# Kernel optimization log

Hardware: AMD Instinct MI355X
Metric: run time of the kernel (lower is better)

The kernel has to match this reference:

```python
import jax, jax.numpy as jnp
import numpy as np

DIM = 20
N = 200000
E = 6400000
ITERATIONS = 3


def setup_inputs() -> dict:
    key = jax.random.key(0)
    ks = jax.random.split(key, 20)
    inp = {
        "h": jax.random.normal(ks[0], (N, DIM), dtype=jnp.float32),
        "node2depth": jax.random.randint(ks[1], (N,), 0, 5, dtype=jnp.int32),
        "edge_src": jax.random.randint(ks[2], (E,), 0, N, dtype=jnp.int32),
        "edge_dst": jax.random.randint(ks[3], (E,), 0, N, dtype=jnp.int32),
    }
    # Six DIM x DIM Linear layers (weight stored [out,in] like torch, plus bias)
    scale = 1.0 / np.sqrt(DIM)
    names = ["Wz", "Uz", "Wr", "Ur", "Wh", "Uh"]
    for j, nm in enumerate(names):
        inp[nm + "_w"] = jax.random.uniform(ks[4 + 2 * j], (DIM, DIM), jnp.float32, -scale, scale)
        inp[nm + "_b"] = jax.random.uniform(ks[5 + 2 * j], (DIM,), jnp.float32, -scale, scale)
    return inp


def _linear(x, w, b):
    return x @ w.T + b


def reference(h, Wz_w, Wz_b, Uz_w, Uz_b, Wr_w, Wr_b, Ur_w, Ur_b,
              Wh_w, Wh_b, Uh_w, Uh_b, node2depth, edge_src, edge_dst):
    active = None
    for i in range(ITERATIONS):
        # active set shrinks as i grows (depth + i <= ITERATIONS)
        active = (node2depth + i) <= ITERATIONS  # [N] bool
        af = active.astype(h.dtype)
        # x[u] = sum over neighbors v of h[v], counting only active src AND active dst
        msg = h[edge_src] * af[edge_src][:, None]          # [E, DIM]
        x = jax.ops.segment_sum(msg, edge_dst, num_segments=N)  # [N, DIM]
        x = x * af[:, None]
        z = jax.nn.sigmoid(_linear(x, Wz_w, Wz_b) + _linear(h, Uz_w, Uz_b))
        r = jax.nn.sigmoid(_linear(x, Wr_w, Wr_b) + _linear(h, Ur_w, Ur_b))
        h_cand = jnp.tanh(_linear(x, Wh_w, Wh_b) + _linear(r * h, Uh_w, Uh_b))
        h_new = z * h + (1.0 - z) * h_cand
        # inactive nodes are dropped from the dict in the original; since the
        # active set only shrinks, keeping their old h is equivalent
        h = jnp.where(active[:, None], h_new, h)
    # original returns only nodes active at the last iteration; zero out the rest
    return jnp.where(active[:, None], h, jnp.zeros_like(h))
```

## Files before the change

kernel.cpp:

```cpp
#include <hip/hip_runtime.h>

#define DIM    20
#define NN     200000
#define EE     6400000
#define ITERS  3
#define BLOCK  256

#define NODES_PER_FINE   64
#define NFINE            3125
#define NCOARSE          98
#define FINE_PER_COARSE  32
#define TILE             4096
#define IPT              16
#define XSTRIDE          21
#define NBINS            2560

typedef unsigned int u32;

__global__ __launch_bounds__(BLOCK) void k1_count(const int* __restrict__ edst,
                                                  int* __restrict__ fine_cnt) {
    __shared__ u32 lhist[NFINE];
    int tid = threadIdx.x;
    for (int i = tid; i < NFINE; i += BLOCK) lhist[i] = 0;
    __syncthreads();
    for (int e = blockIdx.x * BLOCK + tid; e < EE; e += gridDim.x * BLOCK) {
        int d = edst[e];
        atomicAdd(&lhist[d >> 6], 1u);
    }
    __syncthreads();
    for (int i = tid; i < NFINE; i += BLOCK) {
        u32 v = lhist[i];
        if (v) atomicAdd((u32*)&fine_cnt[i], v);
    }
}

__global__ __launch_bounds__(BLOCK) void k2_scan(const int* __restrict__ fine_cnt,
                                                 int* __restrict__ fine_base,
                                                 int* __restrict__ fine_cursor,
                                                 int* __restrict__ coarse_base,
                                                 int* __restrict__ coarse_cursor) {
    const int CH = 13;
    int tid = threadIdx.x;
    int loc[CH];
    int base = tid * CH;
    int s = 0;
    #pragma unroll
    for (int j = 0; j < CH; ++j) {
        int idx = base + j;
        int v = (idx < NFINE) ? fine_cnt[idx] : 0;
        loc[j] = v; s += v;
    }
    __shared__ int wsum[4];
    int lane = tid & 63, wid = tid >> 6;
    int incl = s;
    #pragma unroll
    for (int off = 1; off < 64; off <<= 1) {
        int t = __shfl_up(incl, off, 64);
        if (lane >= off) incl += t;
    }
    if (lane == 63) wsum[wid] = incl;
    __syncthreads();
    int woff = 0;
    for (int w = 0; w < wid; ++w) woff += wsum[w];
    int run = woff + incl - s;
    #pragma unroll
    for (int j = 0; j < CH; ++j) {
        int idx = base + j;
        if (idx < NFINE) {
            fine_base[idx]   = run;
            fine_cursor[idx] = run;
            run += loc[j];
        }
    }
    if (tid == 0) fine_base[NFINE] = EE;
    __syncthreads();
    if (tid < NCOARSE + 1) {
        int f = tid * FINE_PER_COARSE; if (f > NFINE) f = NFINE;
        int v = fine_base[f];
        coarse_base[tid] = v;
        if (tid < NCOARSE) coarse_cursor[tid] = v;
    }
}

__global__ __launch_bounds__(BLOCK) void p1_split(const int* __restrict__ esrc,
                                                  const int* __restrict__ edst,
                                                  const int* __restrict__ depth,
                                                  int* __restrict__ coarse_cursor,
                                                  u32* __restrict__ buf1) {
    __shared__ u32 lhist[NCOARSE];
    __shared__ u32 gbase[NCOARSE];
    int tid = threadIdx.x;
    int start = blockIdx.x * TILE;
    if (tid < NCOARSE) lhist[tid] = 0;
    __syncthreads();

    u32 item[IPT]; u32 key[IPT]; u32 rank[IPT];
    #pragma unroll
    for (int k = 0; k < IPT; ++k) {
        int e = start + k * BLOCK + tid;
        if (e < EE) {
            int d = edst[e];
            int s = esrc[e];
            u32 dep = (u32)depth[s];
            u32 c = (u32)d >> 11;
            key[k]  = c;
            item[k] = ((u32)d & 2047u) | ((u32)s << 11) | (dep << 29);
            rank[k] = atomicAdd(&lhist[c], 1u);
        }
    }
    __syncthreads();
    if (tid < NCOARSE) {
        u32 cnt = lhist[tid];
        gbase[tid] = cnt ? (u32)atomicAdd((u32*)&coarse_cursor[tid], cnt) : 0u;
    }
    __syncthreads();
    #pragma unroll
    for (int k = 0; k < IPT; ++k) {
        int e = start + k * BLOCK + tid;
        if (e < EE) buf1[gbase[key[k]] + rank[k]] = item[k];
    }
}

__global__ __launch_bounds__(BLOCK) void p2_split(const u32* __restrict__ buf1,
                                                  const int* __restrict__ coarse_base,
                                                  int* __restrict__ fine_cursor,
                                                  u32* __restrict__ buf2) {
    __shared__ u32 lhist[2 * FINE_PER_COARSE];
    __shared__ u32 gbase[2 * FINE_PER_COARSE];
    __shared__ int cb[NCOARSE + 1];
    __shared__ int sc0;
    int tid = threadIdx.x;
    int start = blockIdx.x * TILE;
    if (tid < NCOARSE + 1) cb[tid] = coarse_base[tid];
    if (tid < 2 * FINE_PER_COARSE) { lhist[tid] = 0; gbase[tid] = 0; }
    __syncthreads();
    if (tid == 0) {
        int c = 0;
        while (c + 1 < NCOARSE && cb[c + 1] <= start) ++c;
        sc0 = c;
    }
    __syncthreads();
    int c0 = sc0;
    int b1 = cb[c0 + 1];

    u32 item[IPT]; u32 key[IPT]; u32 rank[IPT];
    #pragma unroll
    for (int k = 0; k < IPT; ++k) {
        int i = start + k * BLOCK + tid;
        if (i < EE) {
            u32 w = buf1[i];
            u32 dlow = w & 2047u;
            u32 sdep = w >> 11;
            u32 kk = ((i < b1) ? 0u : (u32)FINE_PER_COARSE) + (dlow >> 6);
            key[k]  = kk;
            item[k] = (dlow & 63u) | (sdep << 6);
            rank[k] = atomicAdd(&lhist[kk], 1u);
        }
    }
    __syncthreads();
    if (tid < 2 * FINE_PER_COARSE) {
        u32 cnt = lhist[tid];
        int idx = c0 * FINE_PER_COARSE + tid;
        if (cnt && idx < NFINE)
            gbase[tid] = (u32)atomicAdd((u32*)&fine_cursor[idx], cnt);
    }
    __syncthreads();
    #pragma unroll
    for (int k = 0; k < IPT; ++k) {
        int i = start + k * BLOCK + tid;
        if (i < EE) buf2[gbase[key[k]] + rank[k]] = item[k];
    }
}

__global__ __launch_bounds__(BLOCK) void pb_sort(const u32* __restrict__ buf2,
                                                 const int* __restrict__ fine_base,
                                                 int* __restrict__ ptr,
                                                 u32* __restrict__ cnt3,
                                                 u32* __restrict__ ssrc) {
    __shared__ u32 hist[NBINS];
    __shared__ u32 ebase[NBINS];
    __shared__ u32 lout[TILE];
    __shared__ u32 wsum[4];
    int tid = threadIdx.x;
    int b = blockIdx.x;
    int lo = fine_base[b];
    int hi = fine_base[b + 1];
    int cnt = hi - lo;
    for (int i = tid; i < NBINS; i += BLOCK) hist[i] = 0;
    __syncthreads();

    u32 item[IPT]; u32 key[IPT]; u32 rank[IPT];
    #pragma unroll
    for (int k = 0; k < IPT; ++k) {
        int i = lo + k * BLOCK + tid;
        if (i < hi) {
            u32 w = buf2[i];
            u32 src = (w >> 6) & 0x3FFFFu;
            u32 kk = (w & 63u) * 40u + (w >> 24) * 8u + (src >> 15);
            key[k]  = kk;
            item[k] = src;
            rank[k] = atomicAdd(&hist[kk], 1u);
        }
    }
    __syncthreads();
    {
        const int CH = 10;
        int base = tid * CH;
        u32 loc[CH];
        u32 s = 0;
        #pragma unroll
        for (int j = 0; j < CH; ++j) { loc[j] = hist[base + j]; s += loc[j]; }
        int lane = tid & 63, wid = tid >> 6;
        u32 incl = s;
        #pragma unroll
        for (int off = 1; off < 64; off <<= 1) {
            u32 t = __shfl_up((int)incl, off, 64);
            if (lane >= off) incl += t;
        }
        if (lane == 63) wsum[wid] = incl;
        __syncthreads();
        u32 woff = 0;
        for (int w = 0; w < wid; ++w) woff += wsum[w];
        u32 run = woff + incl - s;
        #pragma unroll
        for (int j = 0; j < CH; ++j) { ebase[base + j] = run; run += loc[j]; }
    }
    __syncthreads();
    if (tid < NODES_PER_FINE) {
        u32 base0 = ebase[tid * 40];
        u32 c1 = ebase[tid * 40 + 16] - base0;
        u32 c2 = ebase[tid * 40 + 24] - base0;
        u32 c3 = ebase[tid * 40 + 32] - base0;
        int u = b * NODES_PER_FINE + tid;
        ptr[u]  = lo + (int)base0;
        cnt3[u] = c1 | (c2 << 10) | (c3 << 20);
    }
    #pragma unroll
    for (int k = 0; k < IPT; ++k) {
        int i = lo + k * BLOCK + tid;
        if (i < hi) lout[ebase[key[k]] + rank[k]] = item[k];
    }
    __syncthreads();
    for (int j = tid; j < cnt; j += BLOCK) ssrc[lo + j] = lout[j];
}

__device__ __forceinline__ u32 pack_bf16x2(float a, float b) {
    u32 ua = __float_as_uint(a);
    u32 ub = __float_as_uint(b);
    ua = (ua + 0x7FFFu + ((ua >> 16) & 1u)) >> 16;
    ub = (ub + 0x7FFFu + ((ub >> 16) & 1u)) & 0xFFFF0000u;
    return ua | ub;
}

__global__ __launch_bounds__(BLOCK) void hconv(const float* __restrict__ h,
                                               u32* __restrict__ hb) {
    int g = blockIdx.x * BLOCK + threadIdx.x;
    if (g >= NN * 16) return;
    int node = g >> 4, slot = g & 15;
    u32 v = 0;
    if (slot < 10) {
        float2 f = *(const float2*)(h + (size_t)node * DIM + slot * 2);
        v = pack_bf16x2(f.x, f.y);
    }
    hb[g] = v;
}


__device__ __forceinline__ float bl(u32 w) { return __uint_as_float(w << 16); }
__device__ __forceinline__ float bh(u32 w) { return __uint_as_float(w & 0xFFFF0000u); }

__device__ __forceinline__ void acc_bf16row(float* x, uint4 A, uint4 B, uint2 C) {
    x[0]+=bl(A.x);  x[1]+=bh(A.x);  x[2]+=bl(A.y);  x[3]+=bh(A.y);
    x[4]+=bl(A.z);  x[5]+=bh(A.z);  x[6]+=bl(A.w);  x[7]+=bh(A.w);
    x[8]+=bl(B.x);  x[9]+=bh(B.x);  x[10]+=bl(B.y); x[11]+=bh(B.y);
    x[12]+=bl(B.z); x[13]+=bh(B.z); x[14]+=bl(B.w); x[15]+=bh(B.w);
    x[16]+=bl(C.x); x[17]+=bh(C.x); x[18]+=bl(C.y); x[19]+=bh(C.y);
}

__device__ __forceinline__ float fast_sigmoid(float t) {
    return 1.0f / (1.0f + __expf(-t));
}
__device__ __forceinline__ float fast_tanh(float t) {
    t = fminf(fmaxf(t, -15.0f), 15.0f);
    float e2 = __expf(2.0f * t);
    return (e2 - 1.0f) / (e2 + 1.0f);
}

__global__ __launch_bounds__(BLOCK) void grnn_iter(
    const float* __restrict__ h_in, float* __restrict__ h_out,
    const u32* __restrict__ hb_in, u32* __restrict__ hb_out,
    const int* __restrict__ depth, const int* __restrict__ ptr,
    const u32* __restrict__ cnt3, const u32* __restrict__ ssrc,
    const float* __restrict__ Wz, const float* __restrict__ bWz,
    const float* __restrict__ Uz, const float* __restrict__ bUz,
    const float* __restrict__ Wr, const float* __restrict__ bWr,
    const float* __restrict__ Ur, const float* __restrict__ bUr,
    const float* __restrict__ Wh, const float* __restrict__ bWh,
    const float* __restrict__ Uh, const float* __restrict__ bUh,
    int it, int shift, int isFinal)
{
    __shared__ float xl[64 * XSTRIDE];
    int tid = threadIdx.x;
    int nl  = tid >> 2;
    int t   = tid & 3;
    int lim = ITERS - it;

    {
        int u = blockIdx.x * 64 + nl;
        if (depth[u] <= lim) {
            int p = ptr[u];
            int d = (int)((cnt3[u] >> shift) & 1023u);
            float x[DIM];
            #pragma unroll
            for (int k = 0; k < DIM; ++k) x[k] = 0.0f;
            int e = t;
            for (; e + 12 < d; e += 16) {
                u32 v0 = ssrc[p + e];
                u32 v1 = ssrc[p + e + 4];
                u32 v2 = ssrc[p + e + 8];
                u32 v3 = ssrc[p + e + 12];
                const u32* r0 = hb_in + (size_t)v0 * 16;
                const u32* r1 = hb_in + (size_t)v1 * 16;
                const u32* r2 = hb_in + (size_t)v2 * 16;
                const u32* r3 = hb_in + (size_t)v3 * 16;
                uint4 A0 = *(const uint4*)r0; uint4 B0 = *(const uint4*)(r0 + 4);
                uint2 C0 = *(const uint2*)(r0 + 8);
                uint4 A1 = *(const uint4*)r1; uint4 B1 = *(const uint4*)(r1 + 4);
                uint2 C1 = *(const uint2*)(r1 + 8);
                uint4 A2 = *(const uint4*)r2; uint4 B2 = *(const uint4*)(r2 + 4);
                uint2 C2 = *(const uint2*)(r2 + 8);
                uint4 A3 = *(const uint4*)r3; uint4 B3 = *(const uint4*)(r3 + 4);
                uint2 C3 = *(const uint2*)(r3 + 8);
                acc_bf16row(x, A0, B0, C0);
                acc_bf16row(x, A1, B1, C1);
                acc_bf16row(x, A2, B2, C2);
                acc_bf16row(x, A3, B3, C3);
            }
            for (; e < d; e += 4) {
                u32 v0 = ssrc[p + e];
                const u32* r0 = hb_in + (size_t)v0 * 16;
                uint4 A0 = *(const uint4*)r0; uint4 B0 = *(const uint4*)(r0 + 4);
                uint2 C0 = *(const uint2*)(r0 + 8);
                acc_bf16row(x, A0, B0, C0);
            }
            #pragma unroll
            for (int k = 0; k < DIM; ++k) {
                x[k] += __shfl_xor(x[k], 1, 64);
                x[k] += __shfl_xor(x[k], 2, 64);
            }
            float* xr = xl + nl * XSTRIDE;
            #pragma unroll
            for (int q = 0; q < 5; ++q) xr[q * 4 + t] = x[q * 4 + t];
        }
    }
    __syncthreads();
    if (tid >= 64) return;

    int u = blockIdx.x * 64 + tid;
    bool act = depth[u] <= lim;
    if (!act) {
        if (isFinal) {
            float4 z4 = make_float4(0.f, 0.f, 0.f, 0.f);
            float4* o4 = (float4*)(h_out + (size_t)u * DIM);
            #pragma unroll
            for (int q = 0; q < 5; ++q) o4[q] = z4;
        }
        return;
    }

    float x[DIM], h[DIM];
    #pragma unroll
    for (int k = 0; k < DIM; ++k) x[k] = xl[tid * XSTRIDE + k];
    {
        const float4* hv = (const float4*)(h_in + (size_t)u * DIM);
        float4 a0 = hv[0], a1 = hv[1], a2 = hv[2], a3 = hv[3], a4 = hv[4];
        h[0]=a0.x; h[1]=a0.y; h[2]=a0.z; h[3]=a0.w;
        h[4]=a1.x; h[5]=a1.y; h[6]=a1.z; h[7]=a1.w;
        h[8]=a2.x; h[9]=a2.y; h[10]=a2.z; h[11]=a2.w;
        h[12]=a3.x; h[13]=a3.y; h[14]=a3.z; h[15]=a3.w;
        h[16]=a4.x; h[17]=a4.y; h[18]=a4.z; h[19]=a4.w;
    }

    float z[DIM], rh[DIM];
    #pragma unroll
    for (int j = 0; j < DIM; ++j) {
        float sz = bWz[j] + bUz[j];
        float sr = bWr[j] + bUr[j];
        #pragma unroll
        for (int k = 0; k < DIM; ++k) {
            sz += x[k] * Wz[j * DIM + k];
            sz += h[k] * Uz[j * DIM + k];
            sr += x[k] * Wr[j * DIM + k];
            sr += h[k] * Ur[j * DIM + k];
        }
        z[j]  = fast_sigmoid(sz);
        rh[j] = fast_sigmoid(sr) * h[j];
    }

    float o[DIM];
    #pragma unroll
    for (int j = 0; j < DIM; ++j) {
        float sh = bWh[j] + bUh[j];
        #pragma unroll
        for (int k = 0; k < DIM; ++k) {
            sh += x[k]  * Wh[j * DIM + k];
            sh += rh[k] * Uh[j * DIM + k];
        }
        float hc = fast_tanh(sh);
        o[j] = z[j] * h[j] + (1.0f - z[j]) * hc;
    }

    {
        float4* o4 = (float4*)(h_out + (size_t)u * DIM);
        o4[0] = make_float4(o[0],  o[1],  o[2],  o[3]);
        o4[1] = make_float4(o[4],  o[5],  o[6],  o[7]);
        o4[2] = make_float4(o[8],  o[9],  o[10], o[11]);
        o4[3] = make_float4(o[12], o[13], o[14], o[15]);
        o4[4] = make_float4(o[16], o[17], o[18], o[19]);
    }
    if (!isFinal) {
        u32* row = hb_out + (size_t)u * 16;
        uint4 wA = make_uint4(pack_bf16x2(o[0], o[1]),  pack_bf16x2(o[2], o[3]),
                              pack_bf16x2(o[4], o[5]),  pack_bf16x2(o[6], o[7]));
        uint4 wB = make_uint4(pack_bf16x2(o[8], o[9]),  pack_bf16x2(o[10], o[11]),
                              pack_bf16x2(o[12], o[13]), pack_bf16x2(o[14], o[15]));
        uint2 wC = make_uint2(pack_bf16x2(o[16], o[17]), pack_bf16x2(o[18], o[19]));
        *(uint4*)row       = wA;
        *(uint4*)(row + 4) = wB;
        *(uint2*)(row + 8) = wC;
    }
}


extern "C" void kernel_launch(void* const* d_in, const int* in_sizes, int n_in,
                              void* d_out, int out_size, void* d_ws, size_t ws_size,
                              hipStream_t stream) {
    const float* h0    = (const float*)d_in[0];
    const int*   depth = (const int*)d_in[1];
    const int*   esrc  = (const int*)d_in[2];
    const int*   edst  = (const int*)d_in[3];
    const float* Wz  = (const float*)d_in[4];  const float* bWz = (const float*)d_in[5];
    const float* Uz  = (const float*)d_in[6];  const float* bUz = (const float*)d_in[7];
    const float* Wr  = (const float*)d_in[8];  const float* bWr = (const float*)d_in[9];
    const float* Ur  = (const float*)d_in[10]; const float* bUr = (const float*)d_in[11];
    const float* Wh  = (const float*)d_in[12]; const float* bWh = (const float*)d_in[13];
    const float* Uh  = (const float*)d_in[14]; const float* bUh = (const float*)d_in[15];
    float* out = (float*)d_out;

    int* W = (int*)d_ws;
    int*  fine_cnt      = W + 0;
    int*  fine_base     = W + 3200;
    int*  fine_cursor   = W + 6400;
    int*  coarse_base   = W + 9600;
    int*  coarse_cursor = W + 9728;
    int*  ptr           = W + 9856;
    u32*  cnt3          = (u32*)(W + 209920);
    u32*  buf1          = (u32*)(W + 409984);
    u32*  buf2          = buf1 + EE;
    float* h1           = (float*)(buf2 + EE);
    u32*  hbA           = (u32*)(h1 + (size_t)NN * DIM);
    u32*  hbB           = hbA + (size_t)NN * 16;
    u32*  ssrc          = buf1;
    float* h2           = (float*)buf2;

    hipMemsetAsync(fine_cnt, 0, NFINE * sizeof(int), stream);

    int ntile = (EE + TILE - 1) / TILE;

    k1_count<<<256, BLOCK, 0, stream>>>(edst, fine_cnt);
    k2_scan <<<1,   BLOCK, 0, stream>>>(fine_cnt, fine_base, fine_cursor,
                                        coarse_base, coarse_cursor);
    p1_split<<<ntile, BLOCK, 0, stream>>>(esrc, edst, depth, coarse_cursor, buf1);
    p2_split<<<ntile, BLOCK, 0, stream>>>(buf1, coarse_base, fine_cursor, buf2);
    pb_sort <<<NFINE, BLOCK, 0, stream>>>(buf2, fine_base, ptr, cnt3, ssrc);
    hconv   <<<(NN * 16) / BLOCK, BLOCK, 0, stream>>>(h0, hbA);

    grnn_iter<<<NFINE, BLOCK, 0, stream>>>(h0, h1, hbA, hbB, depth, ptr, cnt3, ssrc,
        Wz, bWz, Uz, bUz, Wr, bWr, Ur, bUr, Wh, bWh, Uh, bUh, 0, 20, 0);
    grnn_iter<<<NFINE, BLOCK, 0, stream>>>(h1, h2, hbB, hbA, depth, ptr, cnt3, ssrc,
        Wz, bWz, Uz, bUz, Wr, bWr, Ur, bUr, Wh, bWh, Uh, bUh, 1, 10, 0);
    grnn_iter<<<NFINE, BLOCK, 0, stream>>>(h2, out, hbA, hbB, depth, ptr, cnt3, ssrc,
        Wz, bWz, Uz, bUz, Wr, bWr, Ur, bUr, Wh, bWh, Uh, bUh, 2, 0, 1);
}
```

Baseline: 525.2 us.

## Shard neighbor lists by source range and use two threads per node

```diff
diff --git a/kernel.cpp b/kernel.cpp
--- a/kernel.cpp
+++ b/kernel.cpp
@@ -13,7 +13,8 @@
 #define TILE             4096
 #define IPT              16
 #define XSTRIDE          21
-#define NBINS            2560
+#define NSHARD           4
+#define NBINS            1280
 
 typedef unsigned int u32;
 
@@ -174,8 +175,8 @@
 
 __global__ __launch_bounds__(BLOCK) void pb_sort(const u32* __restrict__ buf2,
                                                  const int* __restrict__ fine_base,
-                                                 int* __restrict__ ptr,
-                                                 u32* __restrict__ cnt3,
+                                                 u32* __restrict__ ptrS,
+                                                 u32* __restrict__ cnt3S,
                                                  u32* __restrict__ ssrc) {
     __shared__ u32 hist[NBINS];
     __shared__ u32 ebase[NBINS];
@@ -196,7 +197,7 @@
         if (i < hi) {
             u32 w = buf2[i];
             u32 src = (w >> 6) & 0x3FFFFu;
-            u32 kk = (w & 63u) * 40u + (w >> 24) * 8u + (src >> 15);
+            u32 kk = (w & 63u) * 20u + (src >> 16) * 5u + (w >> 24);
             key[k]  = kk;
             item[k] = src;
             rank[k] = atomicAdd(&hist[kk], 1u);
@@ -204,7 +205,7 @@
     }
     __syncthreads();
     {
-        const int CH = 10;
+        const int CH = 5;
         int base = tid * CH;
         u32 loc[CH];
         u32 s = 0;
@@ -227,13 +228,17 @@
     }
     __syncthreads();
     if (tid < NODES_PER_FINE) {
-        u32 base0 = ebase[tid * 40];
-        u32 c1 = ebase[tid * 40 + 16] - base0;
-        u32 c2 = ebase[tid * 40 + 24] - base0;
-        u32 c3 = ebase[tid * 40 + 32] - base0;
         int u = b * NODES_PER_FINE + tid;
-        ptr[u]  = lo + (int)base0;
-        cnt3[u] = c1 | (c2 << 10) | (c3 << 20);
+        int base20 = tid * 20;
+        #pragma unroll
+        for (int s = 0; s < NSHARD; ++s) {
+            u32 b0 = ebase[base20 + s * 5];
+            u32 c1 = ebase[base20 + s * 5 + 2] - b0;
+            u32 c2 = ebase[base20 + s * 5 + 3] - b0;
+            u32 c3 = ebase[base20 + s * 5 + 4] - b0;
+            ptrS[u * NSHARD + s]  = (u32)(lo + (int)b0);
+            cnt3S[u * NSHARD + s] = c1 | (c2 << 10) | (c3 << 20);
+        }
     }
     #pragma unroll
     for (int k = 0; k < IPT; ++k) {
@@ -286,11 +291,11 @@
     return (e2 - 1.0f) / (e2 + 1.0f);
 }
 
-__global__ __launch_bounds__(BLOCK) void grnn_iter(
+__global__ __launch_bounds__(BLOCK, 6) void grnn_iter(
     const float* __restrict__ h_in, float* __restrict__ h_out,
     const u32* __restrict__ hb_in, u32* __restrict__ hb_out,
-    const int* __restrict__ depth, const int* __restrict__ ptr,
-    const u32* __restrict__ cnt3, const u32* __restrict__ ssrc,
+    const int* __restrict__ depth, const u32* __restrict__ ptrS,
+    const u32* __restrict__ cnt3S, const u32* __restrict__ ssrc,
     const float* __restrict__ Wz, const float* __restrict__ bWz,
     const float* __restrict__ Uz, const float* __restrict__ bUz,
     const float* __restrict__ Wr, const float* __restrict__ bWr,
@@ -299,64 +304,57 @@
     const float* __restrict__ Uh, const float* __restrict__ bUh,
     int it, int shift, int isFinal)
 {
-    __shared__ float xl[64 * XSTRIDE];
-    int tid = threadIdx.x;
-    int nl  = tid >> 2;
-    int t   = tid & 3;
+    __shared__ float xl[128 * XSTRIDE];
+    int tid = threadIdx.x;
+    int nl  = tid >> 1;
+    int t   = tid & 1;
     int lim = ITERS - it;
 
     {
-        int u = blockIdx.x * 64 + nl;
-        if (depth[u] <= lim) {
-            int p = ptr[u];
-            int d = (int)((cnt3[u] >> shift) & 1023u);
+        int u = blockIdx.x * 128 + nl;
+        if (u < NN && depth[u] <= lim) {
             float x[DIM];
             #pragma unroll
             for (int k = 0; k < DIM; ++k) x[k] = 0.0f;
-            int e = t;
-            for (; e + 12 < d; e += 16) {
-                u32 v0 = ssrc[p + e];
-                u32 v1 = ssrc[p + e + 4];
-                u32 v2 = ssrc[p + e + 8];
-                u32 v3 = ssrc[p + e + 12];
-                const u32* r0 = hb_in + (size_t)v0 * 16;
-                const u32* r1 = hb_in + (size_t)v1 * 16;
-                const u32* r2 = hb_in + (size_t)v2 * 16;
-                const u32* r3 = hb_in + (size_t)v3 * 16;
-                uint4 A0 = *(const uint4*)r0; uint4 B0 = *(const uint4*)(r0 + 4);
-                uint2 C0 = *(const uint2*)(r0 + 8);
-                uint4 A1 = *(const uint4*)r1; uint4 B1 = *(const uint4*)(r1 + 4);
-                uint2 C1 = *(const uint2*)(r1 + 8);
-                uint4 A2 = *(const uint4*)r2; uint4 B2 = *(const uint4*)(r2 + 4);
-                uint2 C2 = *(const uint2*)(r2 + 8);
-                uint4 A3 = *(const uint4*)r3; uint4 B3 = *(const uint4*)(r3 + 4);
-                uint2 C3 = *(const uint2*)(r3 + 8);
-                acc_bf16row(x, A0, B0, C0);
-                acc_bf16row(x, A1, B1, C1);
-                acc_bf16row(x, A2, B2, C2);
-                acc_bf16row(x, A3, B3, C3);
-            }
-            for (; e < d; e += 4) {
-                u32 v0 = ssrc[p + e];
-                const u32* r0 = hb_in + (size_t)v0 * 16;
-                uint4 A0 = *(const uint4*)r0; uint4 B0 = *(const uint4*)(r0 + 4);
-                uint2 C0 = *(const uint2*)(r0 + 8);
-                acc_bf16row(x, A0, B0, C0);
+            const u32* pS = ptrS  + (size_t)u * NSHARD;
+            const u32* cS = cnt3S + (size_t)u * NSHARD;
+            #pragma unroll
+            for (int s = 0; s < NSHARD; ++s) {
+                int p = (int)pS[s];
+                int d = (int)((cS[s] >> shift) & 1023u);
+                int e = t;
+                for (; e + 2 < d; e += 4) {
+                    u32 v0 = ssrc[p + e];
+                    u32 v1 = ssrc[p + e + 2];
+                    const u32* r0 = hb_in + (size_t)v0 * 16;
+                    const u32* r1 = hb_in + (size_t)v1 * 16;
+                    uint4 A0 = *(const uint4*)r0; uint4 B0 = *(const uint4*)(r0 + 4);
+                    uint2 C0 = *(const uint2*)(r0 + 8);
+                    uint4 A1 = *(const uint4*)r1; uint4 B1 = *(const uint4*)(r1 + 4);
+                    uint2 C1 = *(const uint2*)(r1 + 8);
+                    acc_bf16row(x, A0, B0, C0);
+                    acc_bf16row(x, A1, B1, C1);
+                }
+                if (e < d) {
+                    u32 v0 = ssrc[p + e];
+                    const u32* r0 = hb_in + (size_t)v0 * 16;
+                    uint4 A0 = *(const uint4*)r0; uint4 B0 = *(const uint4*)(r0 + 4);
+                    uint2 C0 = *(const uint2*)(r0 + 8);
+                    acc_bf16row(x, A0, B0, C0);
+                }
             }
             #pragma unroll
-            for (int k = 0; k < DIM; ++k) {
-                x[k] += __shfl_xor(x[k], 1, 64);
-                x[k] += __shfl_xor(x[k], 2, 64);
-            }
+            for (int k = 0; k < DIM; ++k) x[k] += __shfl_xor(x[k], 1, 64);
             float* xr = xl + nl * XSTRIDE;
             #pragma unroll
-            for (int q = 0; q < 5; ++q) xr[q * 4 + t] = x[q * 4 + t];
-        }
-    }
-    __syncthreads();
-    if (tid >= 64) return;
-
-    int u = blockIdx.x * 64 + tid;
+            for (int q = 0; q < 10; ++q) xr[q * 2 + t] = x[q * 2 + t];
+        }
+    }
+    __syncthreads();
+    if (tid >= 128) return;
+
+    int u = blockIdx.x * 128 + tid;
+    if (u >= NN) return;
     bool act = depth[u] <= lim;
     if (!act) {
         if (isFinal) {
@@ -453,9 +451,9 @@
     int*  fine_cursor   = W + 6400;
     int*  coarse_base   = W + 9600;
     int*  coarse_cursor = W + 9728;
-    int*  ptr           = W + 9856;
-    u32*  cnt3          = (u32*)(W + 209920);
-    u32*  buf1          = (u32*)(W + 409984);
+    u32*  ptrS          = (u32*)(W + 9856);
+    u32*  cnt3S         = (u32*)(W + 809856);
+    u32*  buf1          = (u32*)(W + 1609856);
     u32*  buf2          = buf1 + EE;
     float* h1           = (float*)(buf2 + EE);
     u32*  hbA           = (u32*)(h1 + (size_t)NN * DIM);
@@ -466,19 +464,20 @@
     hipMemsetAsync(fine_cnt, 0, NFINE * sizeof(int), stream);
 
     int ntile = (EE + TILE - 1) / TILE;
+    int ggrid = (NN + 127) / 128;
 
     k1_count<<<256, BLOCK, 0, stream>>>(edst, fine_cnt);
     k2_scan <<<1,   BLOCK, 0, stream>>>(fine_cnt, fine_base, fine_cursor,
                                         coarse_base, coarse_cursor);
     p1_split<<<ntile, BLOCK, 0, stream>>>(esrc, edst, depth, coarse_cursor, buf1);
     p2_split<<<ntile, BLOCK, 0, stream>>>(buf1, coarse_base, fine_cursor, buf2);
-    pb_sort <<<NFINE, BLOCK, 0, stream>>>(buf2, fine_base, ptr, cnt3, ssrc);
+    pb_sort <<<NFINE, BLOCK, 0, stream>>>(buf2, fine_base, ptrS, cnt3S, ssrc);
     hconv   <<<(NN * 16) / BLOCK, BLOCK, 0, stream>>>(h0, hbA);
 
-    grnn_iter<<<NFINE, BLOCK, 0, stream>>>(h0, h1, hbA, hbB, depth, ptr, cnt3, ssrc,
+    grnn_iter<<<ggrid, BLOCK, 0, stream>>>(h0, h1, hbA, hbB, depth, ptrS, cnt3S, ssrc,
         Wz, bWz, Uz, bUz, Wr, bWr, Ur, bUr, Wh, bWh, Uh, bUh, 0, 20, 0);
-    grnn_iter<<<NFINE, BLOCK, 0, stream>>>(h1, h2, hbB, hbA, depth, ptr, cnt3, ssrc,
+    grnn_iter<<<ggrid, BLOCK, 0, stream>>>(h1, h2, hbB, hbA, depth, ptrS, cnt3S, ssrc,
         Wz, bWz, Uz, bUz, Wr, bWr, Ur, bUr, Wh, bWh, Uh, bUh, 1, 10, 0);
-    grnn_iter<<<NFINE, BLOCK, 0, stream>>>(h2, out, hbA, hbB, depth, ptr, cnt3, ssrc,
+    grnn_iter<<<ggrid, BLOCK, 0, stream>>>(h2, out, hbA, hbB, depth, ptrS, cnt3S, ssrc,
         Wz, bWz, Uz, bUz, Wr, bWr, Ur, bUr, Wh, bWh, Uh, bUh, 2, 0, 1);
 }
```

New measurement: 577.9 us. 1.1x slower.
